# Optimization experiments

Hardware: AMD Instinct MI355X
Metric: run time of the kernel (lower is better)

The kernel has to match this reference:

```python
import jax, jax.numpy as jnp
import numpy as np

INTRINSIC_DIM = 3  # all linear dims, no periodic dims
EPS = 1e-10


def _cdist(a, b):
    # Euclidean distance via the expanded form; clamp for numerical safety.
    sq = (jnp.sum(a * a, axis=1)[:, None]
          + jnp.sum(b * b, axis=1)[None, :]
          - 2.0 * (a @ b.T))
    return jnp.sqrt(jnp.maximum(sq, 0.0))


def _thin_plate_kernel(r, dim):
    r_safe = jnp.maximum(r, EPS)
    if dim == 2:
        k = r_safe ** 2 * jnp.log(r_safe)
    else:
        k = r_safe ** (dim - 2) * jnp.log(r_safe)
    return jnp.where(r < EPS, jnp.zeros_like(k), k)


def setup_inputs() -> dict:
    key = jax.random.key(0)
    k1, k2, k3, k4 = jax.random.split(key, 4)
    batch, n, d, amb = 16384, 4096, INTRINSIC_DIM, 3
    m = 1 + d  # constant + one linear term per (non-periodic) dim
    u = jax.random.uniform(k1, (batch, d), dtype=jnp.float32)
    control_points = jax.random.uniform(k2, (n, d), dtype=jnp.float32)
    rbf_weights = jax.random.normal(k3, (n, amb), dtype=jnp.float32)
    poly_coeffs = jax.random.normal(k4, (m, amb), dtype=jnp.float32)
    return {"u": u, "control_points": control_points,
            "rbf_weights": rbf_weights, "poly_coeffs": poly_coeffs}


def reference(u, control_points, rbf_weights, poly_coeffs):
    # K_query: (batch, n) TPS kernel on pairwise Euclidean distances
    dists = _cdist(u, control_points)
    K_query = _thin_plate_kernel(dists, dim=INTRINSIC_DIM)
    # Polynomial matrix: [1, x] over all linear dims -> (batch, 1 + d)
    P_query = jnp.concatenate([jnp.ones((u.shape[0], 1), dtype=u.dtype), u], axis=1)
    return K_query @ rbf_weights + P_query @ poly_coeffs
```

## Files before the change

kernel.cpp:

```cpp
#include <hip/hip_runtime.h>


#define CHUNK 256
#define BLK 256

__global__ __launch_bounds__(BLK) void tps_kernel(
    const float* __restrict__ u,
    const float* __restrict__ cp,
    const float* __restrict__ w,
    const float* __restrict__ poly,
    float* __restrict__ out,
    int batch, int n)
{
    __shared__ float s_cx[CHUNK], s_cy[CHUNK], s_cz[CHUNK];
    __shared__ float s_wx[CHUNK], s_wy[CHUNK], s_wz[CHUNK];

    const int tid = threadIdx.x;
    const int qi = blockIdx.x * BLK + tid;
    const int j0 = blockIdx.y * CHUNK;
    const int jn = min(CHUNK, n - j0);

    if (tid < jn) {
        const int g = j0 + tid;
        s_cx[tid] = cp[g * 3 + 0];
        s_cy[tid] = cp[g * 3 + 1];
        s_cz[tid] = cp[g * 3 + 2];
        s_wx[tid] = w[g * 3 + 0];
        s_wy[tid] = w[g * 3 + 1];
        s_wz[tid] = w[g * 3 + 2];
    }
    __syncthreads();

    if (qi >= batch) return;

    const float ux = u[qi * 3 + 0];
    const float uy = u[qi * 3 + 1];
    const float uz = u[qi * 3 + 2];

    float ax = 0.f, ay = 0.f, az = 0.f;
    if (blockIdx.y == 0) {
        ax = poly[0] + ux * poly[3] + uy * poly[6] + uz * poly[9];
        ay = poly[1] + ux * poly[4] + uy * poly[7] + uz * poly[10];
        az = poly[2] + ux * poly[5] + uy * poly[8] + uz * poly[11];
    }

    const float C = 0.34657359027997264f;

    if (jn == CHUNK) {
#pragma unroll 8
        for (int j = 0; j < CHUNK; ++j) {
            const float dx = ux - s_cx[j];
            const float dy = uy - s_cy[j];
            const float dz = uz - s_cz[j];
            float r2 = fmaxf(dx * dx + dy * dy + dz * dz, 1e-30f);
            const float k = __builtin_amdgcn_sqrtf(r2) *
                            (C * __builtin_amdgcn_logf(r2));
            ax = fmaf(k, s_wx[j], ax);
            ay = fmaf(k, s_wy[j], ay);
            az = fmaf(k, s_wz[j], az);
        }
    } else {
        for (int j = 0; j < jn; ++j) {
            const float dx = ux - s_cx[j];
            const float dy = uy - s_cy[j];
            const float dz = uz - s_cz[j];
            float r2 = fmaxf(dx * dx + dy * dy + dz * dz, 1e-30f);
            const float k = __builtin_amdgcn_sqrtf(r2) *
                            (C * __builtin_amdgcn_logf(r2));
            ax = fmaf(k, s_wx[j], ax);
            ay = fmaf(k, s_wy[j], ay);
            az = fmaf(k, s_wz[j], az);
        }
    }

    atomicAdd(&out[qi * 3 + 0], ax);
    atomicAdd(&out[qi * 3 + 1], ay);
    atomicAdd(&out[qi * 3 + 2], az);
}

extern "C" void kernel_launch(void* const* d_in, const int* in_sizes, int n_in,
                              void* d_out, int out_size, void* d_ws, size_t ws_size,
                              hipStream_t stream) {
    const float* u    = (const float*)d_in[0];
    const float* cp   = (const float*)d_in[1];
    const float* w    = (const float*)d_in[2];
    const float* poly = (const float*)d_in[3];
    float* out = (float*)d_out;

    const int batch = in_sizes[0] / 3;
    const int n     = in_sizes[1] / 3;

    hipMemsetAsync(d_out, 0, (size_t)out_size * sizeof(float), stream);

    dim3 block(BLK);
    dim3 grid((batch + BLK - 1) / BLK, (n + CHUNK - 1) / CHUNK);
    tps_kernel<<<grid, block, 0, stream>>>(u, cp, w, poly, out, batch, n);
}
```

Measured before the change: 92.75 us.

## Process two queries per thread with packed shared-memory control points

Each thread now evaluates two query points against each control point. The control points and the C-prescaled weights are packed into float4/float2 shared-memory arrays, so each shared load serves two queries and the multiply by C leaves the inner loop. The chunk size is halved to keep the grid large, which doubles the number of atomic adds and blocks along the n axis. If batch were not a multiple of the block size, the q1 load of u could read out of bounds, since that load is not guarded.

```diff
diff --git a/kernel.cpp b/kernel.cpp
--- a/kernel.cpp
+++ b/kernel.cpp
@@ -1,8 +1,9 @@
 #include <hip/hip_runtime.h>
 
 
-#define CHUNK 256
+#define CHUNK 128
 #define BLK 256
+#define QPT 2
 
 __global__ __launch_bounds__(BLK) void tps_kernel(
     const float* __restrict__ u,
@@ -12,70 +13,73 @@
     float* __restrict__ out,
     int batch, int n)
 {
-    __shared__ float s_cx[CHUNK], s_cy[CHUNK], s_cz[CHUNK];
-    __shared__ float s_wx[CHUNK], s_wy[CHUNK], s_wz[CHUNK];
+    __shared__ float4 s_a[CHUNK];
+    __shared__ float2 s_b[CHUNK];
+
+    const float C = 0.34657359027997264f;
 
     const int tid = threadIdx.x;
-    const int qi = blockIdx.x * BLK + tid;
+    const int q0 = blockIdx.x * (BLK * QPT) + tid;
+    const int q1 = q0 + BLK;
     const int j0 = blockIdx.y * CHUNK;
     const int jn = min(CHUNK, n - j0);
 
     if (tid < jn) {
         const int g = j0 + tid;
-        s_cx[tid] = cp[g * 3 + 0];
-        s_cy[tid] = cp[g * 3 + 1];
-        s_cz[tid] = cp[g * 3 + 2];
-        s_wx[tid] = w[g * 3 + 0];
-        s_wy[tid] = w[g * 3 + 1];
-        s_wz[tid] = w[g * 3 + 2];
+        s_a[tid] = make_float4(cp[g * 3 + 0], cp[g * 3 + 1], cp[g * 3 + 2],
+                               C * w[g * 3 + 0]);
+        s_b[tid] = make_float2(C * w[g * 3 + 1], C * w[g * 3 + 2]);
     }
     __syncthreads();
 
-    if (qi >= batch) return;
+    if (q0 >= batch) return;
 
-    const float ux = u[qi * 3 + 0];
-    const float uy = u[qi * 3 + 1];
-    const float uz = u[qi * 3 + 2];
+    const float ux0 = u[q0 * 3 + 0], uy0 = u[q0 * 3 + 1], uz0 = u[q0 * 3 + 2];
+    const float ux1 = u[q1 * 3 + 0], uy1 = u[q1 * 3 + 1], uz1 = u[q1 * 3 + 2];
 
-    float ax = 0.f, ay = 0.f, az = 0.f;
+    float ax0 = 0.f, ay0 = 0.f, az0 = 0.f;
+    float ax1 = 0.f, ay1 = 0.f, az1 = 0.f;
     if (blockIdx.y == 0) {
-        ax = poly[0] + ux * poly[3] + uy * poly[6] + uz * poly[9];
-        ay = poly[1] + ux * poly[4] + uy * poly[7] + uz * poly[10];
-        az = poly[2] + ux * poly[5] + uy * poly[8] + uz * poly[11];
+        ax0 = poly[0] + ux0 * poly[3] + uy0 * poly[6] + uz0 * poly[9];
+        ay0 = poly[1] + ux0 * poly[4] + uy0 * poly[7] + uz0 * poly[10];
+        az0 = poly[2] + ux0 * poly[5] + uy0 * poly[8] + uz0 * poly[11];
+        ax1 = poly[0] + ux1 * poly[3] + uy1 * poly[6] + uz1 * poly[9];
+        ay1 = poly[1] + ux1 * poly[4] + uy1 * poly[7] + uz1 * poly[10];
+        az1 = poly[2] + ux1 * poly[5] + uy1 * poly[8] + uz1 * poly[11];
     }
 
-    const float C = 0.34657359027997264f;
+#pragma unroll 4
+    for (int j = 0; j < jn; ++j) {
+        const float4 A = s_a[j];
+        const float2 B = s_b[j];
 
-    if (jn == CHUNK) {
-#pragma unroll 8
-        for (int j = 0; j < CHUNK; ++j) {
-            const float dx = ux - s_cx[j];
-            const float dy = uy - s_cy[j];
-            const float dz = uz - s_cz[j];
-            float r2 = fmaxf(dx * dx + dy * dy + dz * dz, 1e-30f);
-            const float k = __builtin_amdgcn_sqrtf(r2) *
-                            (C * __builtin_amdgcn_logf(r2));
-            ax = fmaf(k, s_wx[j], ax);
-            ay = fmaf(k, s_wy[j], ay);
-            az = fmaf(k, s_wz[j], az);
-        }
-    } else {
-        for (int j = 0; j < jn; ++j) {
-            const float dx = ux - s_cx[j];
-            const float dy = uy - s_cy[j];
-            const float dz = uz - s_cz[j];
-            float r2 = fmaxf(dx * dx + dy * dy + dz * dz, 1e-30f);
-            const float k = __builtin_amdgcn_sqrtf(r2) *
-                            (C * __builtin_amdgcn_logf(r2));
-            ax = fmaf(k, s_wx[j], ax);
-            ay = fmaf(k, s_wy[j], ay);
-            az = fmaf(k, s_wz[j], az);
-        }
+        const float dx0 = ux0 - A.x;
+        const float dy0 = uy0 - A.y;
+        const float dz0 = uz0 - A.z;
+        float r20 = fmaxf(fmaf(dx0, dx0, fmaf(dy0, dy0, dz0 * dz0)), 1e-30f);
+        const float k0 = __builtin_amdgcn_sqrtf(r20) * __builtin_amdgcn_logf(r20);
+        ax0 = fmaf(k0, A.w, ax0);
+        ay0 = fmaf(k0, B.x, ay0);
+        az0 = fmaf(k0, B.y, az0);
+
+        const float dx1 = ux1 - A.x;
+        const float dy1 = uy1 - A.y;
+        const float dz1 = uz1 - A.z;
+        float r21 = fmaxf(fmaf(dx1, dx1, fmaf(dy1, dy1, dz1 * dz1)), 1e-30f);
+        const float k1 = __builtin_amdgcn_sqrtf(r21) * __builtin_amdgcn_logf(r21);
+        ax1 = fmaf(k1, A.w, ax1);
+        ay1 = fmaf(k1, B.x, ay1);
+        az1 = fmaf(k1, B.y, az1);
     }
 
-    atomicAdd(&out[qi * 3 + 0], ax);
-    atomicAdd(&out[qi * 3 + 1], ay);
-    atomicAdd(&out[qi * 3 + 2], az);
+    atomicAdd(&out[q0 * 3 + 0], ax0);
+    atomicAdd(&out[q0 * 3 + 1], ay0);
+    atomicAdd(&out[q0 * 3 + 2], az0);
+    if (q1 < batch) {
+        atomicAdd(&out[q1 * 3 + 0], ax1);
+        atomicAdd(&out[q1 * 3 + 1], ay1);
+        atomicAdd(&out[q1 * 3 + 2], az1);
+    }
 }
 
 extern "C" void kernel_launch(void* const* d_in, const int* in_sizes, int n_in,
@@ -93,6 +97,6 @@
     hipMemsetAsync(d_out, 0, (size_t)out_size * sizeof(float), stream);
 
     dim3 block(BLK);
-    dim3 grid((batch + BLK - 1) / BLK, (n + CHUNK - 1) / CHUNK);
+    dim3 grid((batch + BLK * QPT - 1) / (BLK * QPT), (n + CHUNK - 1) / CHUNK);
     tps_kernel<<<grid, block, 0, stream>>>(u, cp, w, poly, out, batch, n);
 }
```

Measured after the change: 87.16 us. 6.0% less time.
